# Kernel tuning notes

Hardware: AMD Instinct MI355X
Metric: run time of the kernel (lower is better)

The kernel has to match this reference:

```python
import jax, jax.numpy as jnp
import numpy as np

N_NODES = 50000
N_EDGES = 800000
IN_CH = 16
HIDDEN = [128, 128, 128]
OUT_CH = 16
SELF_LOOP_W = 2.0  # improved=True


def _glorot(key, fan_in, fan_out):
    s = jnp.sqrt(6.0 / (fan_in + fan_out))
    return jax.random.uniform(key, (fan_in, fan_out), jnp.float32, -s, s)


def setup_inputs() -> dict:
    key = jax.random.key(0)
    ks = jax.random.split(key, 12)
    x = jax.random.normal(ks[0], (N_NODES, IN_CH), jnp.float32)
    edge_index = jax.random.randint(ks[1], (2, N_EDGES), 0, N_NODES, jnp.int64)
    edge_attr = jax.random.uniform(ks[2], (N_EDGES,), jnp.float32)
    dims = [IN_CH] + HIDDEN + [OUT_CH]
    inp = {"x": x, "edge_index": edge_index, "edge_attr": edge_attr}
    for i in range(4):
        inp[f"w{i}"] = _glorot(ks[3 + i], dims[i], dims[i + 1])
        inp[f"b{i}"] = jnp.zeros((dims[i + 1],), jnp.float32)
    return inp


def _gcn_norm(edge_index, edge_attr, n):
    # add self-loops with weight 2.0 (improved=True), symmetric normalization
    src = jnp.concatenate([edge_index[0], jnp.arange(n, dtype=edge_index.dtype)])
    dst = jnp.concatenate([edge_index[1], jnp.arange(n, dtype=edge_index.dtype)])
    w = jnp.concatenate([edge_attr, jnp.full((n,), SELF_LOOP_W, edge_attr.dtype)])
    deg = jax.ops.segment_sum(w, dst, num_segments=n)
    dinv = jnp.where(deg > 0, jax.lax.rsqrt(jnp.where(deg > 0, deg, 1.0)), 0.0)
    norm = dinv[src] * w * dinv[dst]
    return src, dst, norm


def _gcn_conv(x, src, dst, norm, w, b, n):
    h = x @ w                                   # [N, out]
    msg = norm[:, None] * h[src]                # gather + scale, [E+N, out]
    return jax.ops.segment_sum(msg, dst, num_segments=n) + b


def reference(x, edge_index, edge_attr, w0, b0, w1, b1, w2, b2, w3, b3):
    n = x.shape[0]
    src, dst, norm = _gcn_norm(edge_index, edge_attr, n)
    ws = [(w0, b0), (w1, b1), (w2, b2), (w3, b3)]
    for i, (w, b) in enumerate(ws):
        x = _gcn_conv(x, src, dst, norm, w, b, n)
        if i < len(ws) - 1:
            x = jax.nn.relu(x)
    return x
```

## Files before the change

### kernel.cpp

```cpp
#include <hip/hip_runtime.h>
#include <hip/hip_fp16.h>


static constexpr int NN = 50000;
static constexpr int NE = 800000;
static constexpr int ROW_U = 80;
static constexpr int NBKT = (NN + 63) / 64;
static constexpr int BCAP = 1280;
static constexpr int EPB = 4096;
static constexpr int NBLK = (NE + EPB - 1) / EPB;

typedef _Float16 half8_t __attribute__((ext_vector_type(8)));
typedef float float4_t __attribute__((ext_vector_type(4)));

union Frag { uint4 u; half8_t h; };
union H2U2 { uint2 u; __half2 h[2]; };
union H4U4 { uint4 u; __half2 h[4]; };

__device__ __forceinline__ float unpack_w(uint e) {
  return __half2float(__ushort_as_half((ushort)(e >> 16)));
}


__global__ void prep_kernel(const float* __restrict__ w1, const float* __restrict__ w2,
                            const float* __restrict__ w3, char* __restrict__ wt1,
                            char* __restrict__ wt2, char* __restrict__ wt3) {
  int t = blockIdx.x * blockDim.x + threadIdx.x;
  if (t < 16384) {
    int k = t >> 7, n = t & 127;
    int off = n * 256 + ((2 * k) ^ ((n & 7) << 4));
    *(ushort*)(wt1 + off) = __half_as_ushort(__float2half(w1[t]));
    *(ushort*)(wt2 + off) = __half_as_ushort(__float2half(w2[t]));
  }
  if (t < 2048) {
    int k = t >> 4, n = t & 15;
    *(ushort*)(wt3 + n * 256 + ((2 * k) ^ ((n & 7) << 4))) = __half_as_ushort(__float2half(w3[t]));
  }
}

__global__ void __launch_bounds__(256) hist_kernel(const int* __restrict__ dst,
                                                   int* __restrict__ blockhist, int ne) {
  __shared__ int bin[NBKT];
  const int b = blockIdx.x, t = threadIdx.x;
  for (int k = t; k < NBKT; k += 256) bin[k] = 0;
  __syncthreads();
  const int e0 = b * EPB, e1 = min(e0 + EPB, ne);
  for (int i = e0 + t; i < e1; i += 256) atomicAdd(&bin[dst[i] >> 6], 1);
  __syncthreads();
  for (int k = t; k < NBKT; k += 256) blockhist[(size_t)k * NBLK + b] = bin[k];
}

__global__ void __launch_bounds__(256) bscan_kernel(int* __restrict__ blockhist,
                                                    int* __restrict__ bucket_total) {
  __shared__ int s[256];
  const int bkt = blockIdx.x, t = threadIdx.x;
  int v = (t < NBLK) ? blockhist[(size_t)bkt * NBLK + t] : 0;
  s[t] = v;
  __syncthreads();
  for (int off = 1; off < 256; off <<= 1) {
    int u = (t >= off) ? s[t - off] : 0;
    __syncthreads();
    s[t] += u;
    __syncthreads();
  }
  if (t < NBLK) blockhist[(size_t)bkt * NBLK + t] = s[t] - v;
  if (t == 255) bucket_total[bkt] = s[255];
}

__global__ void __launch_bounds__(256) scat_kernel(
    const int* __restrict__ src, const int* __restrict__ dst, const float* __restrict__ ea,
    const int* __restrict__ blockbase, uint2* __restrict__ sorted, int ne) {
  __shared__ int lbase[NBKT];
  __shared__ int lbin[NBKT];
  const int b = blockIdx.x, t = threadIdx.x;
  for (int k = t; k < NBKT; k += 256) {
    lbase[k] = blockbase[(size_t)k * NBLK + b];
    lbin[k] = 0;
  }
  __syncthreads();
  const int e0 = b * EPB, e1 = min(e0 + EPB, ne);
  for (int i = e0 + t; i < e1; i += 256) {
    const int d = dst[i];
    const int bkt = d >> 6;
    const int r = atomicAdd(&lbin[bkt], 1);
    const uint entry = ((uint)__half_as_ushort(__float2half(ea[i])) << 16) | (uint)src[i];
    sorted[(size_t)bkt * BCAP + lbase[bkt] + r] = make_uint2((uint)d, entry);
  }
}

__global__ void __launch_bounds__(256) build_kernel(
    const uint2* __restrict__ sorted, const int* __restrict__ bucket_total,
    const float* __restrict__ x, uint* __restrict__ csr, float* __restrict__ dinv,
    __half* __restrict__ xs, int n) {
  __shared__ int lcnt[64], lpos[64];
  __shared__ float ldeg[64], ldinv[64];
  const int bkt = blockIdx.x, t = threadIdx.x;
  if (t < 64) { lcnt[t] = 0; lpos[t] = 0; ldeg[t] = 0.f; }
  __syncthreads();
  const int d0 = bkt * 64;
  const int cn = bucket_total[bkt];
  const uint2* base = sorted + (size_t)bkt * BCAP;
  for (int i = t; i < cn; i += 256) {
    uint2 e = base[i];
    int ld = (int)e.x - d0;
    atomicAdd(&lcnt[ld], 1);
    atomicAdd(&ldeg[ld], unpack_w(e.y));
  }
  __syncthreads();
  if (t < 64 && d0 + t < n) {
    csr[(size_t)(d0 + t) * ROW_U] = (uint)lcnt[t];
    float dn = rsqrtf(2.f + ldeg[t]);
    ldinv[t] = dn;
    dinv[d0 + t] = dn;
  }
  __syncthreads();
  for (int i = t; i < cn; i += 256) {
    uint2 e = base[i];
    int ld = (int)e.x - d0;
    int slot = atomicAdd(&lpos[ld], 1);
    csr[(size_t)e.x * ROW_U + 4 + slot] = e.y;
  }
  {
    const int nd = t >> 2, c4 = t & 3;
    const int node = d0 + nd;
    if (node < n) {
      float dn = ldinv[nd];
      float4 v = ((const float4*)(x + (size_t)node * 16))[c4];
      H2U2 pk;
      pk.h[0] = __float22half2_rn(make_float2(dn * v.x, dn * v.y));
      pk.h[1] = __float22half2_rn(make_float2(dn * v.z, dn * v.w));
      ((uint2*)(xs + (size_t)node * 16))[c4] = pk.u;
    }
  }
}


template <bool FINAL>
__global__ void __launch_bounds__(256) gather16_kernel(
    const __half* __restrict__ g, const uint* __restrict__ csr, const float* __restrict__ dinv,
    const float* __restrict__ bias, void* __restrict__ dest, int n) {
  const int node = blockIdx.x * 64 + (threadIdx.x >> 2);
  const int cg = threadIdx.x & 3;
  if (node >= n) return;
  const uint2* g2 = (const uint2*)g;
  H2U2 self; self.u = g2[(size_t)node * 4 + cg];
  float2 s0 = __half22float2(self.h[0]), s1 = __half22float2(self.h[1]);
  float4 acc = make_float4(2.f * s0.x, 2.f * s0.y, 2.f * s1.x, 2.f * s1.y);

  const uint* row = csr + (size_t)node * ROW_U;
  const int cn = (int)row[0];
  int e = 0;
  for (; e + 4 <= cn; e += 4) {
    uint4 q = *(const uint4*)(row + 4 + e);
    uint ev[4] = {q.x, q.y, q.z, q.w};
    H2U2 v[4];
#pragma unroll
    for (int j = 0; j < 4; ++j) v[j].u = g2[(size_t)(ev[j] & 0xFFFFu) * 4 + cg];
#pragma unroll
    for (int j = 0; j < 4; ++j) {
      float w = unpack_w(ev[j]);
      float2 f0 = __half22float2(v[j].h[0]), f1 = __half22float2(v[j].h[1]);
      acc.x = fmaf(w, f0.x, acc.x); acc.y = fmaf(w, f0.y, acc.y);
      acc.z = fmaf(w, f1.x, acc.z); acc.w = fmaf(w, f1.y, acc.w);
    }
  }
  for (; e < cn; ++e) {
    uint ev = row[4 + e];
    H2U2 v; v.u = g2[(size_t)(ev & 0xFFFFu) * 4 + cg];
    float w = unpack_w(ev);
    float2 f0 = __half22float2(v.h[0]), f1 = __half22float2(v.h[1]);
    acc.x = fmaf(w, f0.x, acc.x); acc.y = fmaf(w, f0.y, acc.y);
    acc.z = fmaf(w, f1.x, acc.z); acc.w = fmaf(w, f1.y, acc.w);
  }
  float dn = dinv[node];
  if (FINAL) {
    float4 bv = ((const float4*)bias)[cg];
    ((float4*)dest)[(size_t)node * 4 + cg] =
        make_float4(dn * acc.x + bv.x, dn * acc.y + bv.y, dn * acc.z + bv.z, dn * acc.w + bv.w);
  } else {
    H2U2 pk;
    pk.h[0] = __float22half2_rn(make_float2(dn * acc.x, dn * acc.y));
    pk.h[1] = __float22half2_rn(make_float2(dn * acc.z, dn * acc.w));
    ((uint2*)dest)[(size_t)node * 4 + cg] = pk.u;
  }
}

__global__ void __launch_bounds__(256) gather128_kernel(
    const __half* __restrict__ g, const uint* __restrict__ csr, const float* __restrict__ dinv,
    const float* __restrict__ bias, __half* __restrict__ aggh, int n) {
  const int node = blockIdx.x * 16 + (threadIdx.x >> 4);
  const int cg = threadIdx.x & 15;
  if (node >= n) return;
  const uint4* g4 = (const uint4*)g;
  float acc[8];
  {
    H4U4 self; self.u = g4[(size_t)node * 16 + cg];
    float2 f0 = __half22float2(self.h[0]), f1 = __half22float2(self.h[1]);
    float2 f2 = __half22float2(self.h[2]), f3 = __half22float2(self.h[3]);
    acc[0] = 2.f * f0.x; acc[1] = 2.f * f0.y; acc[2] = 2.f * f1.x; acc[3] = 2.f * f1.y;
    acc[4] = 2.f * f2.x; acc[5] = 2.f * f2.y; acc[6] = 2.f * f3.x; acc[7] = 2.f * f3.y;
  }
  const uint* row = csr + (size_t)node * ROW_U;
  const int cn = (int)row[0];
  int e = 0;
  for (; e + 4 <= cn; e += 4) {
    uint4 q = *(const uint4*)(row + 4 + e);
    uint ev[4] = {q.x, q.y, q.z, q.w};
    H4U4 v[4];
#pragma unroll
    for (int j = 0; j < 4; ++j) v[j].u = g4[(size_t)(ev[j] & 0xFFFFu) * 16 + cg];
#pragma unroll
    for (int j = 0; j < 4; ++j) {
      float w = unpack_w(ev[j]);
      float2 f0 = __half22float2(v[j].h[0]), f1 = __half22float2(v[j].h[1]);
      float2 f2 = __half22float2(v[j].h[2]), f3 = __half22float2(v[j].h[3]);
      acc[0] = fmaf(w, f0.x, acc[0]); acc[1] = fmaf(w, f0.y, acc[1]);
      acc[2] = fmaf(w, f1.x, acc[2]); acc[3] = fmaf(w, f1.y, acc[3]);
      acc[4] = fmaf(w, f2.x, acc[4]); acc[5] = fmaf(w, f2.y, acc[5]);
      acc[6] = fmaf(w, f3.x, acc[6]); acc[7] = fmaf(w, f3.y, acc[7]);
    }
  }
  for (; e < cn; ++e) {
    uint ev = row[4 + e];
    H4U4 v; v.u = g4[(size_t)(ev & 0xFFFFu) * 16 + cg];
    float w = unpack_w(ev);
    float2 f0 = __half22float2(v.h[0]), f1 = __half22float2(v.h[1]);
    float2 f2 = __half22float2(v.h[2]), f3 = __half22float2(v.h[3]);
    acc[0] = fmaf(w, f0.x, acc[0]); acc[1] = fmaf(w, f0.y, acc[1]);
    acc[2] = fmaf(w, f1.x, acc[2]); acc[3] = fmaf(w, f1.y, acc[3]);
    acc[4] = fmaf(w, f2.x, acc[4]); acc[5] = fmaf(w, f2.y, acc[5]);
    acc[6] = fmaf(w, f3.x, acc[6]); acc[7] = fmaf(w, f3.y, acc[7]);
  }
  const float dn = dinv[node];
  const float4* b4 = (const float4*)bias;
  float4 bl = b4[cg * 2], bh = b4[cg * 2 + 1];
  float r[8];
  r[0] = fmaxf(dn * acc[0] + bl.x, 0.f); r[1] = fmaxf(dn * acc[1] + bl.y, 0.f);
  r[2] = fmaxf(dn * acc[2] + bl.z, 0.f); r[3] = fmaxf(dn * acc[3] + bl.w, 0.f);
  r[4] = fmaxf(dn * acc[4] + bh.x, 0.f); r[5] = fmaxf(dn * acc[5] + bh.y, 0.f);
  r[6] = fmaxf(dn * acc[6] + bh.z, 0.f); r[7] = fmaxf(dn * acc[7] + bh.w, 0.f);
  H4U4 pk;
  pk.h[0] = __float22half2_rn(make_float2(r[0], r[1]));
  pk.h[1] = __float22half2_rn(make_float2(r[2], r[3]));
  pk.h[2] = __float22half2_rn(make_float2(r[4], r[5]));
  pk.h[3] = __float22half2_rn(make_float2(r[6], r[7]));
  ((uint4*)aggh)[(size_t)node * 16 + cg] = pk.u;
}


__global__ void __launch_bounds__(256) mfma128x128_kernel(
    const __half* __restrict__ Ah, const char* __restrict__ wt,
    const float* __restrict__ dinv, __half* __restrict__ outg, int n) {
  __shared__ char wts[32768];
  for (int i = threadIdx.x; i < 2048; i += 256)
    ((uint4*)wts)[i] = ((const uint4*)wt)[i];
  __syncthreads();
  const int row0 = blockIdx.x * 64;
  const int wave = threadIdx.x >> 6, lane = threadIdx.x & 63;
  const int lr = lane & 15, hi = lane >> 4;
  const int rowL = wave * 16 + lr;
  const char* Arow = (const char*)(Ah + (size_t)(row0 + rowL) * 128);
  const int sw = (lr & 7) << 4;
  float4_t acc[8];
#pragma unroll
  for (int ct = 0; ct < 8; ++ct) acc[ct] = (float4_t){0.f, 0.f, 0.f, 0.f};
#pragma unroll
  for (int k0 = 0; k0 < 128; k0 += 32) {
    const int kb = 2 * k0 + hi * 8;
    uint2 alo = *(const uint2*)(Arow + kb);
    uint2 ahi2 = *(const uint2*)(Arow + kb + 32);
    Frag a; a.u = make_uint4(alo.x, alo.y, ahi2.x, ahi2.y);
#pragma unroll
    for (int ct = 0; ct < 8; ++ct) {
      const char* brow = wts + (ct * 16 + lr) * 256;
      uint2 blo = *(const uint2*)(brow + (kb ^ sw));
      uint2 bhi2 = *(const uint2*)(brow + ((kb + 32) ^ sw));
      Frag b; b.u = make_uint4(blo.x, blo.y, bhi2.x, bhi2.y);
      acc[ct] = __builtin_amdgcn_mfma_f32_16x16x32_f16(a.h, b.h, acc[ct], 0, 0, 0);
    }
  }
  int rr[4]; float dnv[4];
#pragma unroll
  for (int reg = 0; reg < 4; ++reg) {
    rr[reg] = row0 + wave * 16 + hi * 4 + reg;
    dnv[reg] = (rr[reg] < n) ? dinv[rr[reg]] : 0.f;
  }
#pragma unroll
  for (int ct = 0; ct < 8; ++ct) {
    int c = ct * 16 + lr;
#pragma unroll
    for (int reg = 0; reg < 4; ++reg)
      if (rr[reg] < n)
        outg[(size_t)rr[reg] * 128 + c] = __float2half(dnv[reg] * acc[ct][reg]);
  }
}

__global__ void __launch_bounds__(256) mfma128x16_kernel(
    const __half* __restrict__ Ah, const char* __restrict__ wt,
    const float* __restrict__ dinv, __half* __restrict__ outg, int n) {
  __shared__ char wts[4096];
  if (threadIdx.x < 256) ((uint4*)wts)[threadIdx.x] = ((const uint4*)wt)[threadIdx.x];
  __syncthreads();
  const int row0 = blockIdx.x * 64;
  const int wave = threadIdx.x >> 6, lane = threadIdx.x & 63;
  const int lr = lane & 15, hi = lane >> 4;
  const int rowL = wave * 16 + lr;
  const char* Arow = (const char*)(Ah + (size_t)(row0 + rowL) * 128);
  const int sw = (lr & 7) << 4;
  const char* brow = wts + lr * 256;
  float4_t acc = (float4_t){0.f, 0.f, 0.f, 0.f};
#pragma unroll
  for (int k0 = 0; k0 < 128; k0 += 32) {
    const int kb = 2 * k0 + hi * 8;
    uint2 alo = *(const uint2*)(Arow + kb);
    uint2 ahi2 = *(const uint2*)(Arow + kb + 32);
    Frag a; a.u = make_uint4(alo.x, alo.y, ahi2.x, ahi2.y);
    uint2 blo = *(const uint2*)(brow + (kb ^ sw));
    uint2 bhi2 = *(const uint2*)(brow + ((kb + 32) ^ sw));
    Frag b; b.u = make_uint4(blo.x, blo.y, bhi2.x, bhi2.y);
    acc = __builtin_amdgcn_mfma_f32_16x16x32_f16(a.h, b.h, acc, 0, 0, 0);
  }
#pragma unroll
  for (int reg = 0; reg < 4; ++reg) {
    int r = row0 + wave * 16 + hi * 4 + reg;
    if (r < n) outg[(size_t)r * 16 + lr] = __float2half(dinv[r] * acc[reg]);
  }
}

__global__ void __launch_bounds__(256) fused_l0l1_kernel(
    const __half* __restrict__ A16h, const float* __restrict__ w0, const float* __restrict__ b0,
    const char* __restrict__ wt1, const float* __restrict__ dinv, __half* __restrict__ g1, int n) {
  __shared__ float a0[64][17];
  __shared__ float ws0[16 * 128];
  __shared__ float bs0[128];
  __shared__ char wts[32768];
  __shared__ char x1s[16384];
  const int row0 = blockIdx.x * 64;
  for (int i = threadIdx.x; i < 2048; i += 256)
    ((uint4*)wts)[i] = ((const uint4*)wt1)[i];
  for (int i = threadIdx.x; i < 512; i += 256)
    ((float4*)ws0)[i] = ((const float4*)w0)[i];
  if (threadIdx.x < 128) bs0[threadIdx.x] = b0[threadIdx.x];
  {
    int r = threadIdx.x >> 2, c8 = threadIdx.x & 3;
    H2U2 v; v.u = make_uint2(0u, 0u);
    if (row0 + r < n) v.u = ((const uint2*)(A16h + (size_t)(row0 + r) * 16))[c8];
    float2 f0 = __half22float2(v.h[0]), f1 = __half22float2(v.h[1]);
    a0[r][c8 * 4 + 0] = f0.x; a0[r][c8 * 4 + 1] = f0.y;
    a0[r][c8 * 4 + 2] = f1.x; a0[r][c8 * 4 + 3] = f1.y;
  }
  __syncthreads();

  {
    const int rg = threadIdx.x >> 4;
    const int c0 = (threadIdx.x & 15) << 3;
    float acc1[4][8];
#pragma unroll
    for (int i = 0; i < 4; ++i)
#pragma unroll
      for (int j = 0; j < 8; ++j) acc1[i][j] = bs0[c0 + j];
#pragma unroll
    for (int k = 0; k < 16; ++k) {
      float A0 = a0[rg * 4 + 0][k], A1 = a0[rg * 4 + 1][k];
      float A2 = a0[rg * 4 + 2][k], A3 = a0[rg * 4 + 3][k];
#pragma unroll
      for (int j = 0; j < 8; ++j) {
        float b = ws0[k * 128 + c0 + j];
        acc1[0][j] = fmaf(A0, b, acc1[0][j]);
        acc1[1][j] = fmaf(A1, b, acc1[1][j]);
        acc1[2][j] = fmaf(A2, b, acc1[2][j]);
        acc1[3][j] = fmaf(A3, b, acc1[3][j]);
      }
    }
#pragma unroll
    for (int i = 0; i < 4; ++i) {
      int row = rg * 4 + i;
      int swz = (row & 7) << 4;
#pragma unroll
      for (int jp = 0; jp < 4; ++jp) {
        int j = jp * 2;
        __half2 h = __float22half2_rn(make_float2(fmaxf(acc1[i][j], 0.f), fmaxf(acc1[i][j + 1], 0.f)));
        *(uint*)(x1s + row * 256 + ((2 * (c0 + j)) ^ swz)) = *(uint*)&h;
      }
    }
  }
  __syncthreads();

  const int wave = threadIdx.x >> 6, lane = threadIdx.x & 63;
  const int lr = lane & 15, hi = lane >> 4;
  const int rowL = wave * 16 + lr;
  const char* Arow = x1s + rowL * 256;
  const int swa = (rowL & 7) << 4;
  const int swb = (lr & 7) << 4;
  float4_t acc[8];
#pragma unroll
  for (int ct = 0; ct < 8; ++ct) acc[ct] = (float4_t){0.f, 0.f, 0.f, 0.f};
#pragma unroll
  for (int k0 = 0; k0 < 128; k0 += 32) {
    const int kb = 2 * k0 + hi * 8;
    uint2 alo = *(const uint2*)(Arow + (kb ^ swa));
    uint2 ahi2 = *(const uint2*)(Arow + ((kb + 32) ^ swa));
    Frag a; a.u = make_uint4(alo.x, alo.y, ahi2.x, ahi2.y);
#pragma unroll
    for (int ct = 0; ct < 8; ++ct) {
      const char* brow = wts + (ct * 16 + lr) * 256;
      uint2 blo = *(const uint2*)(brow + (kb ^ swb));
      uint2 bhi2 = *(const uint2*)(brow + ((kb + 32) ^ swb));
      Frag b; b.u = make_uint4(blo.x, blo.y, bhi2.x, bhi2.y);
      acc[ct] = __builtin_amdgcn_mfma_f32_16x16x32_f16(a.h, b.h, acc[ct], 0, 0, 0);
    }
  }
  int rr[4]; float dnv[4];
#pragma unroll
  for (int reg = 0; reg < 4; ++reg) {
    rr[reg] = row0 + wave * 16 + hi * 4 + reg;
    dnv[reg] = (rr[reg] < n) ? dinv[rr[reg]] : 0.f;
  }
#pragma unroll
  for (int ct = 0; ct < 8; ++ct) {
    int c = ct * 16 + lr;
#pragma unroll
    for (int reg = 0; reg < 4; ++reg)
      if (rr[reg] < n)
        g1[(size_t)rr[reg] * 128 + c] = __float2half(dnv[reg] * acc[ct][reg]);
  }
}


extern "C" void kernel_launch(void* const* d_in, const int* in_sizes, int n_in,
                              void* d_out, int out_size, void* d_ws, size_t ws_size,
                              hipStream_t stream) {
  const float* x  = (const float*)d_in[0];
  const int*   ei = (const int*)d_in[1];
  const float* ea = (const float*)d_in[2];
  const float* w0 = (const float*)d_in[3];
  const float* b0 = (const float*)d_in[4];
  const float* w1 = (const float*)d_in[5];
  const float* b1 = (const float*)d_in[6];
  const float* w2 = (const float*)d_in[7];
  const float* b2 = (const float*)d_in[8];
  const float* w3 = (const float*)d_in[9];
  const float* b3 = (const float*)d_in[10];
  float* out = (float*)d_out;

  const int* src = ei;
  const int* dst = ei + NE;

  __half* Ah    = (__half*)d_ws;
  __half* gbuf  = Ah + (size_t)NN * 128;
  float*  dinv  = (float*)(gbuf + (size_t)NN * 128);
  char*   wt1   = (char*)(dinv + ((NN + 63) & ~63));
  char*   wt2   = wt1 + 32768;
  char*   wt3   = wt2 + 32768;
  uint*   csr   = (uint*)(wt3 + 4096);
  uint2*  sorted = (uint2*)(csr + (size_t)NN * ROW_U);
  int*    blockhist = (int*)(sorted + (size_t)NBKT * BCAP);
  int*    bucket_total = blockhist + ((NBKT * NBLK + 15) & ~15);

  const int B = 256;
  const int gb64 = (NN + 63) / 64;

  prep_kernel<<<64, B, 0, stream>>>(w1, w2, w3, wt1, wt2, wt3);
  hist_kernel<<<NBLK, B, 0, stream>>>(dst, blockhist, NE);
  bscan_kernel<<<NBKT, B, 0, stream>>>(blockhist, bucket_total);
  scat_kernel<<<NBLK, B, 0, stream>>>(src, dst, ea, blockhist, sorted, NE);
  build_kernel<<<NBKT, B, 0, stream>>>(sorted, bucket_total, x, csr, dinv, gbuf, NN);

  gather16_kernel<false><<<(NN + 63) / 64, B, 0, stream>>>(gbuf, csr, dinv, nullptr, Ah, NN);
  fused_l0l1_kernel<<<gb64, B, 0, stream>>>(Ah, w0, b0, wt1, dinv, gbuf, NN);

  gather128_kernel<<<(NN + 15) / 16, B, 0, stream>>>(gbuf, csr, dinv, b1, Ah, NN);
  mfma128x128_kernel<<<gb64, B, 0, stream>>>(Ah, wt2, dinv, gbuf, NN);

  gather128_kernel<<<(NN + 15) / 16, B, 0, stream>>>(gbuf, csr, dinv, b2, Ah, NN);
  mfma128x16_kernel<<<gb64, B, 0, stream>>>(Ah, wt3, dinv, gbuf, NN);

  gather16_kernel<true><<<(NN + 63) / 64, B, 0, stream>>>(gbuf, csr, dinv, b3, out, NN);
}
```

Baseline: 173.8 us.

## Merge prep into hist kernel, drop scan kernel, unroll gather128 by eight

Folds the weight-prep kernel into the histogram kernel and removes the separate block-scan kernel. The scatter kernel now computes each block's bucket base by summing earlier blocks' histograms, and the build kernel reduces bucket totals itself. The histogram layout is transposed to block-major to suit these reads. The 128-wide gather loop also processes eight neighbors per iteration to keep more loads in flight. This saves two launches, but scat_kernel now does O(NBLK) serial reads per bucket per block, and the wider unroll raises register pressure.

```diff
diff --git a/kernel.cpp b/kernel.cpp
--- a/kernel.cpp
+++ b/kernel.cpp
@@ -22,60 +22,46 @@
 }
 
 
-__global__ void prep_kernel(const float* __restrict__ w1, const float* __restrict__ w2,
-                            const float* __restrict__ w3, char* __restrict__ wt1,
-                            char* __restrict__ wt2, char* __restrict__ wt3) {
-  int t = blockIdx.x * blockDim.x + threadIdx.x;
-  if (t < 16384) {
-    int k = t >> 7, n = t & 127;
-    int off = n * 256 + ((2 * k) ^ ((n & 7) << 4));
-    *(ushort*)(wt1 + off) = __half_as_ushort(__float2half(w1[t]));
-    *(ushort*)(wt2 + off) = __half_as_ushort(__float2half(w2[t]));
-  }
-  if (t < 2048) {
-    int k = t >> 4, n = t & 15;
-    *(ushort*)(wt3 + n * 256 + ((2 * k) ^ ((n & 7) << 4))) = __half_as_ushort(__float2half(w3[t]));
-  }
-}
-
-__global__ void __launch_bounds__(256) hist_kernel(const int* __restrict__ dst,
-                                                   int* __restrict__ blockhist, int ne) {
-  __shared__ int bin[NBKT];
-  const int b = blockIdx.x, t = threadIdx.x;
-  for (int k = t; k < NBKT; k += 256) bin[k] = 0;
-  __syncthreads();
-  const int e0 = b * EPB, e1 = min(e0 + EPB, ne);
-  for (int i = e0 + t; i < e1; i += 256) atomicAdd(&bin[dst[i] >> 6], 1);
-  __syncthreads();
-  for (int k = t; k < NBKT; k += 256) blockhist[(size_t)k * NBLK + b] = bin[k];
-}
-
-__global__ void __launch_bounds__(256) bscan_kernel(int* __restrict__ blockhist,
-                                                    int* __restrict__ bucket_total) {
-  __shared__ int s[256];
-  const int bkt = blockIdx.x, t = threadIdx.x;
-  int v = (t < NBLK) ? blockhist[(size_t)bkt * NBLK + t] : 0;
-  s[t] = v;
-  __syncthreads();
-  for (int off = 1; off < 256; off <<= 1) {
-    int u = (t >= off) ? s[t - off] : 0;
+__global__ void __launch_bounds__(256) hist_prep_kernel(
+    const int* __restrict__ dst, int* __restrict__ blockhist,
+    const float* __restrict__ w1, const float* __restrict__ w2, const float* __restrict__ w3,
+    char* __restrict__ wt1, char* __restrict__ wt2, char* __restrict__ wt3, int ne) {
+  if (blockIdx.x < NBLK) {
+    __shared__ int bin[NBKT];
+    const int b = blockIdx.x, t = threadIdx.x;
+    for (int k = t; k < NBKT; k += 256) bin[k] = 0;
     __syncthreads();
-    s[t] += u;
+    const int e0 = b * EPB, e1 = min(e0 + EPB, ne);
+    for (int i = e0 + t; i < e1; i += 256) atomicAdd(&bin[dst[i] >> 6], 1);
     __syncthreads();
-  }
-  if (t < NBLK) blockhist[(size_t)bkt * NBLK + t] = s[t] - v;
-  if (t == 255) bucket_total[bkt] = s[255];
+    for (int k = t; k < NBKT; k += 256) blockhist[(size_t)b * NBKT + k] = bin[k];
+  } else {
+    const int t = (blockIdx.x - NBLK) * 256 + threadIdx.x;
+    if (t < 16384) {
+      int k = t >> 7, n = t & 127;
+      int off = n * 256 + ((2 * k) ^ ((n & 7) << 4));
+      *(ushort*)(wt1 + off) = __half_as_ushort(__float2half(w1[t]));
+      *(ushort*)(wt2 + off) = __half_as_ushort(__float2half(w2[t]));
+    }
+    if (t < 2048) {
+      int k = t >> 4, n = t & 15;
+      *(ushort*)(wt3 + n * 256 + ((2 * k) ^ ((n & 7) << 4))) = __half_as_ushort(__float2half(w3[t]));
+    }
+  }
 }
 
 __global__ void __launch_bounds__(256) scat_kernel(
     const int* __restrict__ src, const int* __restrict__ dst, const float* __restrict__ ea,
-    const int* __restrict__ blockbase, uint2* __restrict__ sorted, int ne) {
+    const int* __restrict__ blockhist, uint2* __restrict__ sorted, int ne) {
   __shared__ int lbase[NBKT];
   __shared__ int lbin[NBKT];
   const int b = blockIdx.x, t = threadIdx.x;
+  for (int k = t; k < NBKT; k += 256) { lbase[k] = 0; lbin[k] = 0; }
+  __syncthreads();
   for (int k = t; k < NBKT; k += 256) {
-    lbase[k] = blockbase[(size_t)k * NBLK + b];
-    lbin[k] = 0;
+    int s = 0;
+    for (int b2 = 0; b2 < b; ++b2) s += blockhist[(size_t)b2 * NBKT + k];
+    lbase[k] = s;
   }
   __syncthreads();
   const int e0 = b * EPB, e1 = min(e0 + EPB, ne);
@@ -89,16 +75,25 @@
 }
 
 __global__ void __launch_bounds__(256) build_kernel(
-    const uint2* __restrict__ sorted, const int* __restrict__ bucket_total,
+    const uint2* __restrict__ sorted, const int* __restrict__ blockhist,
     const float* __restrict__ x, uint* __restrict__ csr, float* __restrict__ dinv,
     __half* __restrict__ xs, int n) {
   __shared__ int lcnt[64], lpos[64];
   __shared__ float ldeg[64], ldinv[64];
+  __shared__ int red[256];
+  __shared__ int cn_sh;
   const int bkt = blockIdx.x, t = threadIdx.x;
   if (t < 64) { lcnt[t] = 0; lpos[t] = 0; ldeg[t] = 0.f; }
+  red[t] = (t < NBLK) ? blockhist[(size_t)t * NBKT + bkt] : 0;
+  __syncthreads();
+  for (int off = 128; off > 0; off >>= 1) {
+    if (t < off) red[t] += red[t + off];
+    __syncthreads();
+  }
+  if (t == 0) cn_sh = red[0];
   __syncthreads();
   const int d0 = bkt * 64;
-  const int cn = bucket_total[bkt];
+  const int cn = cn_sh;
   const uint2* base = sorted + (size_t)bkt * BCAP;
   for (int i = t; i < cn; i += 256) {
     uint2 e = base[i];
@@ -203,6 +198,24 @@
   const uint* row = csr + (size_t)node * ROW_U;
   const int cn = (int)row[0];
   int e = 0;
+  for (; e + 8 <= cn; e += 8) {
+    uint4 q0 = *(const uint4*)(row + 4 + e);
+    uint4 q1 = *(const uint4*)(row + 8 + e);
+    uint ev[8] = {q0.x, q0.y, q0.z, q0.w, q1.x, q1.y, q1.z, q1.w};
+    H4U4 v[8];
+#pragma unroll
+    for (int j = 0; j < 8; ++j) v[j].u = g4[(size_t)(ev[j] & 0xFFFFu) * 16 + cg];
+#pragma unroll
+    for (int j = 0; j < 8; ++j) {
+      float w = unpack_w(ev[j]);
+      float2 f0 = __half22float2(v[j].h[0]), f1 = __half22float2(v[j].h[1]);
+      float2 f2 = __half22float2(v[j].h[2]), f3 = __half22float2(v[j].h[3]);
+      acc[0] = fmaf(w, f0.x, acc[0]); acc[1] = fmaf(w, f0.y, acc[1]);
+      acc[2] = fmaf(w, f1.x, acc[2]); acc[3] = fmaf(w, f1.y, acc[3]);
+      acc[4] = fmaf(w, f2.x, acc[4]); acc[5] = fmaf(w, f2.y, acc[5]);
+      acc[6] = fmaf(w, f3.x, acc[6]); acc[7] = fmaf(w, f3.y, acc[7]);
+    }
+  }
   for (; e + 4 <= cn; e += 4) {
     uint4 q = *(const uint4*)(row + 4 + e);
     uint ev[4] = {q.x, q.y, q.z, q.w};
@@ -455,16 +468,13 @@
   uint*   csr   = (uint*)(wt3 + 4096);
   uint2*  sorted = (uint2*)(csr + (size_t)NN * ROW_U);
   int*    blockhist = (int*)(sorted + (size_t)NBKT * BCAP);
-  int*    bucket_total = blockhist + ((NBKT * NBLK + 15) & ~15);
 
   const int B = 256;
   const int gb64 = (NN + 63) / 64;
 
-  prep_kernel<<<64, B, 0, stream>>>(w1, w2, w3, wt1, wt2, wt3);
-  hist_kernel<<<NBLK, B, 0, stream>>>(dst, blockhist, NE);
-  bscan_kernel<<<NBKT, B, 0, stream>>>(blockhist, bucket_total);
+  hist_prep_kernel<<<NBLK + 64, B, 0, stream>>>(dst, blockhist, w1, w2, w3, wt1, wt2, wt3, NE);
   scat_kernel<<<NBLK, B, 0, stream>>>(src, dst, ea, blockhist, sorted, NE);
-  build_kernel<<<NBKT, B, 0, stream>>>(sorted, bucket_total, x, csr, dinv, gbuf, NN);
+  build_kernel<<<NBKT, B, 0, stream>>>(sorted, blockhist, x, csr, dinv, gbuf, NN);
 
   gather16_kernel<false><<<(NN + 63) / 64, B, 0, stream>>>(gbuf, csr, dinv, nullptr, Ah, NN);
   fused_l0l1_kernel<<<gb64, B, 0, stream>>>(Ah, w0, b0, wt1, dinv, gbuf, NN);
```

After: 226.1 us. 1.3x slower.
